# Performance work log

Hardware: AMD Instinct MI355X
Metric: run time of the kernel (lower is better)

Reference implementation:

```python
import jax, jax.numpy as jnp
import numpy as np


def _avgpool(x, k):
    # x: (N, C, H, W), k divides H and W
    if k == 1:
        return x
    N, C, H, W = x.shape
    return x.reshape(N, C, H // k, k, W // k, k).mean(axis=(3, 5))


def _pairwise_sum(mu1, var1, mu2, var2):
    # mu*, var*: (N, D). Broadcast to (N, N, D), fused elementwise chain + full sum.
    d = mu1[:, None, :] - mu2[None, :, :]
    v = var1[:, None, :] + var2[None, :, :]
    return jnp.sum(jnp.exp(-0.5 * d * d / v) / jnp.sqrt(v))


def setup_inputs() -> dict:
    key = jax.random.key(0)
    k1, k2, k3, k4 = jax.random.split(key, 4)
    shape = (64, 16, 64, 64)
    return {
        "mu_a": jax.random.normal(k1, shape, dtype=jnp.float32),
        "logvar_a": jax.random.normal(k2, shape, dtype=jnp.float32),
        "mu_b": jax.random.normal(k3, shape, dtype=jnp.float32),
        "logvar_b": jax.random.normal(k4, shape, dtype=jnp.float32),
        "kern": 2,
    }


def reference(mu_a, logvar_a, mu_b, logvar_b, kern):
    k2 = float(kern * kern)
    mu_a_p = _avgpool(mu_a, kern)
    mu_b_p = _avgpool(mu_b, kern)
    var_a = _avgpool(jnp.exp(logvar_a), kern) / k2
    var_b = _avgpool(jnp.exp(logvar_b), kern) / k2

    N = mu_a_p.shape[0]
    mu_a_f = mu_a_p.reshape(N, -1)
    mu_b_f = mu_b_p.reshape(N, -1)
    var_a_f = var_a.reshape(N, -1)
    var_b_f = var_b.reshape(N, -1)

    vaa = _pairwise_sum(mu_a_f, var_a_f, mu_a_f, var_a_f)
    vab = _pairwise_sum(mu_a_f, var_a_f, mu_b_f, var_b_f)
    vbb = _pairwise_sum(mu_b_f, var_b_f, mu_b_f, var_b_f)
    return vaa + vbb - 2.0 * vab
```

## Files before the change

kernel.cpp:

```cpp
#include <hip/hip_runtime.h>

#define N_ 64
#define C_ 16
#define H_ 64
#define W_ 64

#define TRI_BLOCKS 288
#define PAIR_BLOCKS (2 * TRI_BLOCKS + 512)


__global__ __launch_bounds__(256) void pool_kernel(
    const float* __restrict__ mu_a, const float* __restrict__ lv_a,
    const float* __restrict__ mu_b, const float* __restrict__ lv_b,
    const int* __restrict__ kern_p, float* __restrict__ ws,
    float* __restrict__ out) {
    if (blockIdx.x == 0 && threadIdx.x == 0) out[0] = 0.0f;

    const int k = kern_p[0];
    const float LOG2E = 1.44269504088896f;

    if (k == 2) {
        const int Np = (N_ * C_ * H_ * W_) >> 2;
        const int Q  = Np >> 2;
        const int total = 4 * Q;
        for (int g = blockIdx.x * blockDim.x + threadIdx.x; g < total;
             g += gridDim.x * blockDim.x) {
            const int a  = g >> 18;
            const int r4 = g & (Q - 1);
            const int pw4 = (r4 & 7) << 2;
            const int t   = r4 >> 3;
            const int ph  = t & 31;
            const int nc  = t >> 5;
            const float* src = (a == 0) ? mu_a : (a == 1) ? lv_a : (a == 2) ? mu_b : lv_b;
            const bool is_var = (a & 1);
            const float* p0 = src + nc * (H_ * W_) + (ph * 2) * W_ + pw4 * 2;
            float4 r0a = *(const float4*)(p0);
            float4 r0b = *(const float4*)(p0 + 4);
            float4 r1a = *(const float4*)(p0 + W_);
            float4 r1b = *(const float4*)(p0 + W_ + 4);
            float o0, o1, o2, o3;
            if (is_var) {
#define E_(x) __builtin_amdgcn_exp2f((x) * LOG2E)
                o0 = E_(r0a.x) + E_(r0a.y) + E_(r1a.x) + E_(r1a.y);
                o1 = E_(r0a.z) + E_(r0a.w) + E_(r1a.z) + E_(r1a.w);
                o2 = E_(r0b.x) + E_(r0b.y) + E_(r1b.x) + E_(r1b.y);
                o3 = E_(r0b.z) + E_(r0b.w) + E_(r1b.z) + E_(r1b.w);
#undef E_
                const float s = 1.0f / 16.0f;
                o0 *= s; o1 *= s; o2 *= s; o3 *= s;
            } else {
                o0 = r0a.x + r0a.y + r1a.x + r1a.y;
                o1 = r0a.z + r0a.w + r1a.z + r1a.w;
                o2 = r0b.x + r0b.y + r1b.x + r1b.y;
                o3 = r0b.z + r0b.w + r1b.z + r1b.w;
                const float s = 0.25f;
                o0 *= s; o1 *= s; o2 *= s; o3 *= s;
            }
            *(float4*)(ws + (size_t)a * Np + (size_t)r4 * 4) = make_float4(o0, o1, o2, o3);
        }
    } else {
        const int Hp = H_ / k, Wp = W_ / k;
        const int Np = N_ * C_ * Hp * Wp;
        const float inv_k2 = 1.0f / (float)(k * k);
        const float inv_k4 = inv_k2 * inv_k2;
        const int total = 4 * Np;
        for (int p = blockIdx.x * blockDim.x + threadIdx.x; p < total;
             p += gridDim.x * blockDim.x) {
            const int a  = p / Np;
            const int r  = p - a * Np;
            const int pw = r % Wp;
            const int t1 = r / Wp;
            const int ph = t1 % Hp;
            const int nc = t1 / Hp;
            const float* src = (a == 0) ? mu_a : (a == 1) ? lv_a : (a == 2) ? mu_b : lv_b;
            const bool is_var = (a & 1);
            const int base = nc * (H_ * W_) + (ph * k) * W_ + (pw * k);
            float s = 0.0f;
            for (int dy = 0; dy < k; ++dy) {
                const float* row = src + base + dy * W_;
                for (int dx = 0; dx < k; ++dx) {
                    float x = row[dx];
                    s += is_var ? __builtin_amdgcn_exp2f(x * LOG2E) : x;
                }
            }
            ws[(size_t)a * Np + r] = s * (is_var ? inv_k4 : inv_k2);
        }
    }
}

__global__ __launch_bounds__(256) void pair_kernel(const float* __restrict__ ws,
                                                   const int* __restrict__ kern_p,
                                                   float* __restrict__ out) {
    const int k = kern_p[0];
    const int D  = C_ * (H_ / k) * (W_ / k);
    const int Np = N_ * D;

    const float* mu_a = ws;
    const float* va   = ws + (size_t)Np;
    const float* mu_b = ws + (size_t)2 * Np;
    const float* vb   = ws + (size_t)3 * Np;

    const int b = blockIdx.x;
    int set, i, jt;
    if (b >= 2 * TRI_BLOCKS) {
        set = 2;
        const int t = b - 2 * TRI_BLOCKS;
        i  = t >> 3;
        jt = t & 7;
    } else {
        set = (b >= TRI_BLOCKS) ? 1 : 0;
        const int t = (b >= TRI_BLOCKS) ? (b - TRI_BLOCKS) : b;
        int g = 0;
        while (g < 7 && 4 * (g + 1) * (g + 2) <= t) ++g;
        const int r = t - 4 * g * (g + 1);
        i  = 8 * g + r / (g + 1);
        jt = r % (g + 1);
    }

    const float *mu1, *v1, *mu2, *v2;
    if (set == 0)      { mu1 = mu2 = mu_a; v1 = v2 = va; }
    else if (set == 1) { mu1 = mu2 = mu_b; v1 = v2 = vb; }
    else               { mu1 = mu_a; v1 = va; mu2 = mu_b; v2 = vb; }

    const int j0 = jt * 8;
    float wgt[8];
    for (int j8 = 0; j8 < 8; ++j8) {
        if (set == 2) wgt[j8] = -2.0f;
        else {
            const int j = j0 + j8;
            wgt[j8] = (j > i) ? 0.0f : (j == i) ? 1.0f : 2.0f;
        }
    }

    const float NHALF_LOG2E = -0.721347520444482f;
#define TERM(mx1, sx1, mx2, sx2)                                         \
    {                                                                    \
        float v  = (sx1) + (sx2);                                        \
        float rs = __builtin_amdgcn_rsqf(v);                             \
        float d  = (mx1) - (mx2);                                        \
        float e  = __builtin_amdgcn_exp2f(NHALF_LOG2E * (d * d) * (rs * rs)); \
        a += e * rs;                                                     \
    }

    const float* Mi = mu1 + (size_t)i * D;
    const float* Vi = v1  + (size_t)i * D;
    float accs[8] = {0, 0, 0, 0, 0, 0, 0, 0};

    if (D == 16384) {
        const int t4 = threadIdx.x << 2;
        for (int c = 0; c < 4; ++c) {
            const int base = (c << 12) + t4;
            const float4 im0 = *(const float4*)(Mi + base);
            const float4 im1 = *(const float4*)(Mi + base + 1024);
            const float4 im2 = *(const float4*)(Mi + base + 2048);
            const float4 im3 = *(const float4*)(Mi + base + 3072);
            const float4 iv0 = *(const float4*)(Vi + base);
            const float4 iv1 = *(const float4*)(Vi + base + 1024);
            const float4 iv2 = *(const float4*)(Vi + base + 2048);
            const float4 iv3 = *(const float4*)(Vi + base + 3072);
            for (int j8 = 0; j8 < 8; ++j8) {
                const float* Mj = mu2 + (size_t)(j0 + j8) * D + base;
                const float* Vj = v2  + (size_t)(j0 + j8) * D + base;
                const float4 jm0 = *(const float4*)(Mj);
                const float4 jm1 = *(const float4*)(Mj + 1024);
                const float4 jm2 = *(const float4*)(Mj + 2048);
                const float4 jm3 = *(const float4*)(Mj + 3072);
                const float4 jv0 = *(const float4*)(Vj);
                const float4 jv1 = *(const float4*)(Vj + 1024);
                const float4 jv2 = *(const float4*)(Vj + 2048);
                const float4 jv3 = *(const float4*)(Vj + 3072);
                float a = 0.0f;
                TERM(im0.x, iv0.x, jm0.x, jv0.x) TERM(im0.y, iv0.y, jm0.y, jv0.y)
                TERM(im0.z, iv0.z, jm0.z, jv0.z) TERM(im0.w, iv0.w, jm0.w, jv0.w)
                TERM(im1.x, iv1.x, jm1.x, jv1.x) TERM(im1.y, iv1.y, jm1.y, jv1.y)
                TERM(im1.z, iv1.z, jm1.z, jv1.z) TERM(im1.w, iv1.w, jm1.w, jv1.w)
                TERM(im2.x, iv2.x, jm2.x, jv2.x) TERM(im2.y, iv2.y, jm2.y, jv2.y)
                TERM(im2.z, iv2.z, jm2.z, jv2.z) TERM(im2.w, iv2.w, jm2.w, jv2.w)
                TERM(im3.x, iv3.x, jm3.x, jv3.x) TERM(im3.y, iv3.y, jm3.y, jv3.y)
                TERM(im3.z, iv3.z, jm3.z, jv3.z) TERM(im3.w, iv3.w, jm3.w, jv3.w)
                accs[j8] += a;
            }
        }
    } else {
        for (int j8 = 0; j8 < 8; ++j8) {
            const float* Mj = mu2 + (size_t)(j0 + j8) * D;
            const float* Vj = v2  + (size_t)(j0 + j8) * D;
            float a = 0.0f;
            for (int e = threadIdx.x; e < D; e += 256) {
                TERM(Mi[e], Vi[e], Mj[e], Vj[e])
            }
            accs[j8] = a;
        }
    }
#undef TERM

    float tot = 0.0f;
    for (int j8 = 0; j8 < 8; ++j8) tot += wgt[j8] * accs[j8];

    for (int off = 32; off > 0; off >>= 1)
        tot += __shfl_down(tot, off, 64);
    __shared__ float wsum[4];
    const int lane = threadIdx.x & 63;
    const int wid  = threadIdx.x >> 6;
    if (lane == 0) wsum[wid] = tot;
    __syncthreads();
    if (threadIdx.x == 0) {
        atomicAdd(out, wsum[0] + wsum[1] + wsum[2] + wsum[3]);
    }
}

extern "C" void kernel_launch(void* const* d_in, const int* in_sizes, int n_in,
                              void* d_out, int out_size, void* d_ws, size_t ws_size,
                              hipStream_t stream) {
    const float* mu_a = (const float*)d_in[0];
    const float* lv_a = (const float*)d_in[1];
    const float* mu_b = (const float*)d_in[2];
    const float* lv_b = (const float*)d_in[3];
    const int*   kern = (const int*)d_in[4];
    float* out = (float*)d_out;
    float* ws  = (float*)d_ws;

    pool_kernel<<<2048, 256, 0, stream>>>(mu_a, lv_a, mu_b, lv_b, kern, ws, out);
    pair_kernel<<<PAIR_BLOCKS, 256, 0, stream>>>(ws, kern, out);
}
```

Baseline: 166.1 us.

## Split pair-kernel D dimension across four blocks and raise occupancy

```diff
diff --git a/kernel.cpp b/kernel.cpp
--- a/kernel.cpp
+++ b/kernel.cpp
@@ -6,7 +6,9 @@
 #define W_ 64
 
 #define TRI_BLOCKS 288
-#define PAIR_BLOCKS (2 * TRI_BLOCKS + 512)
+#define PAIR_GROUPS (2 * TRI_BLOCKS + 512)
+#define DSPLIT 4
+#define PAIR_BLOCKS (PAIR_GROUPS * DSPLIT)
 
 
 __global__ __launch_bounds__(256) void pool_kernel(
@@ -88,9 +90,9 @@
     }
 }
 
-__global__ __launch_bounds__(256) void pair_kernel(const float* __restrict__ ws,
-                                                   const int* __restrict__ kern_p,
-                                                   float* __restrict__ out) {
+__global__ __launch_bounds__(256, 8) void pair_kernel(const float* __restrict__ ws,
+                                                      const int* __restrict__ kern_p,
+                                                      float* __restrict__ out) {
     const int k = kern_p[0];
     const int D  = C_ * (H_ / k) * (W_ / k);
     const int Np = N_ * D;
@@ -100,16 +102,17 @@
     const float* mu_b = ws + (size_t)2 * Np;
     const float* vb   = ws + (size_t)3 * Np;
 
-    const int b = blockIdx.x;
+    const int pb = blockIdx.x >> 2;
+    const int c  = blockIdx.x & 3;
     int set, i, jt;
-    if (b >= 2 * TRI_BLOCKS) {
+    if (pb >= 2 * TRI_BLOCKS) {
         set = 2;
-        const int t = b - 2 * TRI_BLOCKS;
+        const int t = pb - 2 * TRI_BLOCKS;
         i  = t >> 3;
         jt = t & 7;
     } else {
-        set = (b >= TRI_BLOCKS) ? 1 : 0;
-        const int t = (b >= TRI_BLOCKS) ? (b - TRI_BLOCKS) : b;
+        set = (pb >= TRI_BLOCKS) ? 1 : 0;
+        const int t = (pb >= TRI_BLOCKS) ? (pb - TRI_BLOCKS) : pb;
         int g = 0;
         while (g < 7 && 4 * (g + 1) * (g + 2) <= t) ++g;
         const int r = t - 4 * g * (g + 1);
@@ -133,60 +136,61 @@
     }
 
     const float NHALF_LOG2E = -0.721347520444482f;
-#define TERM(mx1, sx1, mx2, sx2)                                         \
-    {                                                                    \
-        float v  = (sx1) + (sx2);                                        \
-        float rs = __builtin_amdgcn_rsqf(v);                             \
-        float d  = (mx1) - (mx2);                                        \
-        float e  = __builtin_amdgcn_exp2f(NHALF_LOG2E * (d * d) * (rs * rs)); \
-        a += e * rs;                                                     \
-    }
-
-    const float* Mi = mu1 + (size_t)i * D;
-    const float* Vi = v1  + (size_t)i * D;
+#define TERM(mx1, sx1, mx2, sx2)                                       \
+    {                                                                  \
+        float v  = (sx1) + (sx2);                                      \
+        float rs = __builtin_amdgcn_rsqf(v);                           \
+        float d  = (mx1) - (mx2);                                      \
+        float t_ = d * rs;                                             \
+        float e  = __builtin_amdgcn_exp2f((NHALF_LOG2E * t_) * t_);    \
+        a = fmaf(e, rs, a);                                            \
+    }
+
     float accs[8] = {0, 0, 0, 0, 0, 0, 0, 0};
 
     if (D == 16384) {
-        const int t4 = threadIdx.x << 2;
-        for (int c = 0; c < 4; ++c) {
-            const int base = (c << 12) + t4;
-            const float4 im0 = *(const float4*)(Mi + base);
-            const float4 im1 = *(const float4*)(Mi + base + 1024);
-            const float4 im2 = *(const float4*)(Mi + base + 2048);
-            const float4 im3 = *(const float4*)(Mi + base + 3072);
-            const float4 iv0 = *(const float4*)(Vi + base);
-            const float4 iv1 = *(const float4*)(Vi + base + 1024);
-            const float4 iv2 = *(const float4*)(Vi + base + 2048);
-            const float4 iv3 = *(const float4*)(Vi + base + 3072);
-            for (int j8 = 0; j8 < 8; ++j8) {
-                const float* Mj = mu2 + (size_t)(j0 + j8) * D + base;
-                const float* Vj = v2  + (size_t)(j0 + j8) * D + base;
-                const float4 jm0 = *(const float4*)(Mj);
-                const float4 jm1 = *(const float4*)(Mj + 1024);
-                const float4 jm2 = *(const float4*)(Mj + 2048);
-                const float4 jm3 = *(const float4*)(Mj + 3072);
-                const float4 jv0 = *(const float4*)(Vj);
-                const float4 jv1 = *(const float4*)(Vj + 1024);
-                const float4 jv2 = *(const float4*)(Vj + 2048);
-                const float4 jv3 = *(const float4*)(Vj + 3072);
-                float a = 0.0f;
-                TERM(im0.x, iv0.x, jm0.x, jv0.x) TERM(im0.y, iv0.y, jm0.y, jv0.y)
-                TERM(im0.z, iv0.z, jm0.z, jv0.z) TERM(im0.w, iv0.w, jm0.w, jv0.w)
-                TERM(im1.x, iv1.x, jm1.x, jv1.x) TERM(im1.y, iv1.y, jm1.y, jv1.y)
-                TERM(im1.z, iv1.z, jm1.z, jv1.z) TERM(im1.w, iv1.w, jm1.w, jv1.w)
-                TERM(im2.x, iv2.x, jm2.x, jv2.x) TERM(im2.y, iv2.y, jm2.y, jv2.y)
-                TERM(im2.z, iv2.z, jm2.z, jv2.z) TERM(im2.w, iv2.w, jm2.w, jv2.w)
-                TERM(im3.x, iv3.x, jm3.x, jv3.x) TERM(im3.y, iv3.y, jm3.y, jv3.y)
-                TERM(im3.z, iv3.z, jm3.z, jv3.z) TERM(im3.w, iv3.w, jm3.w, jv3.w)
-                accs[j8] += a;
-            }
+        const int base = (c << 12) + (threadIdx.x << 2);
+        const float* Mi = mu1 + (size_t)i * D + base;
+        const float* Vi = v1  + (size_t)i * D + base;
+        const float4 im0 = *(const float4*)(Mi);
+        const float4 im1 = *(const float4*)(Mi + 1024);
+        const float4 im2 = *(const float4*)(Mi + 2048);
+        const float4 im3 = *(const float4*)(Mi + 3072);
+        const float4 iv0 = *(const float4*)(Vi);
+        const float4 iv1 = *(const float4*)(Vi + 1024);
+        const float4 iv2 = *(const float4*)(Vi + 2048);
+        const float4 iv3 = *(const float4*)(Vi + 3072);
+        for (int j8 = 0; j8 < 8; ++j8) {
+            const float* Mj = mu2 + (size_t)(j0 + j8) * D + base;
+            const float* Vj = v2  + (size_t)(j0 + j8) * D + base;
+            const float4 jm0 = *(const float4*)(Mj);
+            const float4 jm1 = *(const float4*)(Mj + 1024);
+            const float4 jm2 = *(const float4*)(Mj + 2048);
+            const float4 jm3 = *(const float4*)(Mj + 3072);
+            const float4 jv0 = *(const float4*)(Vj);
+            const float4 jv1 = *(const float4*)(Vj + 1024);
+            const float4 jv2 = *(const float4*)(Vj + 2048);
+            const float4 jv3 = *(const float4*)(Vj + 3072);
+            float a = 0.0f;
+            TERM(im0.x, iv0.x, jm0.x, jv0.x) TERM(im0.y, iv0.y, jm0.y, jv0.y)
+            TERM(im0.z, iv0.z, jm0.z, jv0.z) TERM(im0.w, iv0.w, jm0.w, jv0.w)
+            TERM(im1.x, iv1.x, jm1.x, jv1.x) TERM(im1.y, iv1.y, jm1.y, jv1.y)
+            TERM(im1.z, iv1.z, jm1.z, jv1.z) TERM(im1.w, iv1.w, jm1.w, jv1.w)
+            TERM(im2.x, iv2.x, jm2.x, jv2.x) TERM(im2.y, iv2.y, jm2.y, jv2.y)
+            TERM(im2.z, iv2.z, jm2.z, jv2.z) TERM(im2.w, iv2.w, jm2.w, jv2.w)
+            TERM(im3.x, iv3.x, jm3.x, jv3.x) TERM(im3.y, iv3.y, jm3.y, jv3.y)
+            TERM(im3.z, iv3.z, jm3.z, jv3.z) TERM(im3.w, iv3.w, jm3.w, jv3.w)
+            accs[j8] += a;
         }
     } else {
+        const int lo = (c * D) >> 2, hi = ((c + 1) * D) >> 2;
+        const float* Mi = mu1 + (size_t)i * D;
+        const float* Vi = v1  + (size_t)i * D;
         for (int j8 = 0; j8 < 8; ++j8) {
             const float* Mj = mu2 + (size_t)(j0 + j8) * D;
             const float* Vj = v2  + (size_t)(j0 + j8) * D;
             float a = 0.0f;
-            for (int e = threadIdx.x; e < D; e += 256) {
+            for (int e = lo + (int)threadIdx.x; e < hi; e += 256) {
                 TERM(Mi[e], Vi[e], Mj[e], Vj[e])
             }
             accs[j8] = a;
@@ -220,6 +224,6 @@
     float* out = (float*)d_out;
     float* ws  = (float*)d_ws;
 
-    pool_kernel<<<2048, 256, 0, stream>>>(mu_a, lv_a, mu_b, lv_b, kern, ws, out);
+    pool_kernel<<<4096, 256, 0, stream>>>(mu_a, lv_a, mu_b, lv_b, kern, ws, out);
     pair_kernel<<<PAIR_BLOCKS, 256, 0, stream>>>(ws, kern, out);
 }
```

Measured after the change: 248.2 us. +49.4%, slower.
